# Kernel tuning notes

Measured on AMD Instinct MI355X. Metric: run time of the kernel, lower is better.

## Reference

```python
import jax, jax.numpy as jnp
import numpy as np

N = 100_000      # num_nodes
E = 1_600_000    # num_edges (avg degree 16)
D = 64           # embedding_dim
L = 3            # num_layers


def setup_inputs() -> dict:
    key = jax.random.key(0)
    k1, k2 = jax.random.split(key)
    edge_index = jax.random.randint(k1, (2, E), 0, N, dtype=jnp.int64)
    edge_weight = jnp.ones((E,), jnp.float32)
    # nn.init.normal_(std=0.1)
    embedding = 0.1 * jax.random.normal(k2, (N, D), dtype=jnp.float32)
    return {"embedding": embedding, "edge_weight": edge_weight, "edge_index": edge_index}


def reference(embedding, edge_weight, edge_index):
    n = embedding.shape[0]
    self_idx = jnp.arange(n, dtype=edge_index.dtype)
    # add_self_loops: append (i, i) with weight 1 (PyG default fill_value)
    row = jnp.concatenate([edge_index[0], self_idx])  # source j
    col = jnp.concatenate([edge_index[1], self_idx])  # target i
    ew = jnp.concatenate([edge_weight, jnp.ones((n,), embedding.dtype)])
    # degree() counts occurrences of row (unweighted)
    deg = jax.ops.segment_sum(jnp.ones_like(ew), row, num_segments=n)
    deg_inv_sqrt = jnp.where(deg > 0, jax.lax.rsqrt(deg), 0.0)
    norm = deg_inv_sqrt[row] * ew * deg_inv_sqrt[col]  # [E+N]

    x = embedding
    acc = embedding  # running sum of layer-0..L embeddings
    for _ in range(L):
        # gather from source, scale, scatter-add to target (dropout off in eval)
        msg = norm[:, None] * x[row]                       # [E+N, D]
        x = jax.ops.segment_sum(msg, col, num_segments=n)  # [N, D]
        acc = acc + x
    return acc / (L + 1)
```

## Files before the change

### kernel.cpp

```cpp
#include <hip/hip_runtime.h>
#include <stdint.h>

#define DIM 64
#define BINS 20000
#define RANGES 5
#define NSLICE 51
#define TBH 512
#define SCAN_TILE 1024

__device__ __forceinline__ unsigned bf16rne(float f) {
    unsigned u = __float_as_uint(f);
    return (u + 0x7FFFu + ((u >> 16) & 1u)) >> 16;
}
__device__ __forceinline__ unsigned pack2(float lo, float hi) {
    return bf16rne(lo) | (bf16rne(hi) << 16);
}
#define UNPK(u, lo, hi) { lo = __uint_as_float((u) << 16); hi = __uint_as_float((u) & 0xFFFF0000u); }

__global__ void __launch_bounds__(TBH)
hist_kernel(const int* __restrict__ src, const int* __restrict__ dst,
            int* __restrict__ partialsA, int* __restrict__ partialsB,
            int* __restrict__ lrank, int E, int N, int Es) {
    __shared__ int h[BINS];
    const int b = blockIdx.x;
    const int kind = b / (RANGES * NSLICE);
    const int rs = b % (RANGES * NSLICE);
    const int r = rs / NSLICE, s = rs % NSLICE;
    const int base = r * BINS;
    const int hi = min(base + BINS, N);
    const int nb = hi - base;
    for (int j = threadIdx.x; j < nb; j += TBH) h[j] = 0;
    __syncthreads();
    const int e0 = s * Es, e1 = min(e0 + Es, E);
    if (kind == 0) {
#pragma unroll 4
        for (int i = e0 + threadIdx.x; i < e1; i += TBH) {
            unsigned j = (unsigned)(dst[i] - base);
            if (j < (unsigned)BINS) lrank[i] = atomicAdd(&h[j], 1);
        }
    } else {
#pragma unroll 4
        for (int i = e0 + threadIdx.x; i < e1; i += TBH) {
            unsigned j = (unsigned)(src[i] - base);
            if (j < (unsigned)BINS) atomicAdd(&h[j], 1);
        }
    }
    __syncthreads();
    int* part = (kind ? partialsB : partialsA) + (size_t)s * N + base;
    for (int j = threadIdx.x; j < nb; j += TBH) part[j] = h[j];
}

__global__ void __launch_bounds__(256)
merge_kernel(int* __restrict__ partialsA, const int* __restrict__ partialsB,
             int* __restrict__ indeg, float* __restrict__ dis, int N) {
    const int i = blockIdx.x * blockDim.x + threadIdx.x;
    if (i >= N) return;
    int run = 0;
    for (int s = 0; s < NSLICE; ++s) {
        int v = partialsA[(size_t)s * N + i];
        partialsA[(size_t)s * N + i] = run;
        run += v;
    }
    indeg[i] = run;
    int od = 0;
    for (int s = 0; s < NSLICE; ++s) od += partialsB[(size_t)s * N + i];
    dis[i] = rsqrtf((float)od + 1.0f);
}


__global__ void __launch_bounds__(256)
scan_partial(const int* __restrict__ indeg, int* __restrict__ partial, int n) {
    __shared__ int wsum[4];
    const int tid = threadIdx.x;
    const int base = blockIdx.x * SCAN_TILE + tid * 4;
    int s = 0;
    if (base + 3 < n) {
        int4 v = *(const int4*)(indeg + base);
        s = v.x + v.y + v.z + v.w;
    } else {
        for (int i = 0; i < 4; ++i) if (base + i < n) s += indeg[base + i];
    }
    for (int off = 32; off > 0; off >>= 1) s += __shfl_down(s, off, 64);
    const int lane = tid & 63, wid = tid >> 6;
    if (lane == 0) wsum[wid] = s;
    __syncthreads();
    if (tid == 0) partial[blockIdx.x] = wsum[0] + wsum[1] + wsum[2] + wsum[3];
}

__global__ void scan_blocksums(int* __restrict__ partial, int* __restrict__ offsets,
                               int nblocks, int n) {
    __shared__ int buf[1024];
    const int t = threadIdx.x;
    int v = (t < nblocks) ? partial[t] : 0;
    buf[t] = v;
    __syncthreads();
    for (int off = 1; off < 1024; off <<= 1) {
        int add = (t >= off) ? buf[t - off] : 0;
        __syncthreads();
        buf[t] += add;
        __syncthreads();
    }
    if (t < nblocks) partial[t] = buf[t] - v;
    if (t == 1023) offsets[n] = buf[1023];
}

__global__ void __launch_bounds__(256)
scan_final(const int* __restrict__ indeg, const int* __restrict__ partial,
           int* __restrict__ offsets, int n) {
    __shared__ int wpre[4];
    const int tid = threadIdx.x;
    const int base = blockIdx.x * SCAN_TILE + tid * 4;
    int v0 = 0, v1 = 0, v2 = 0, v3 = 0;
    if (base + 3 < n) {
        int4 v = *(const int4*)(indeg + base);
        v0 = v.x; v1 = v.y; v2 = v.z; v3 = v.w;
    } else {
        if (base + 0 < n) v0 = indeg[base + 0];
        if (base + 1 < n) v1 = indeg[base + 1];
        if (base + 2 < n) v2 = indeg[base + 2];
        if (base + 3 < n) v3 = indeg[base + 3];
    }
    const int s = v0 + v1 + v2 + v3;
    int inc = s;
    const int lane = tid & 63, wid = tid >> 6;
    for (int off = 1; off < 64; off <<= 1) {
        int t = __shfl_up(inc, off, 64);
        if (lane >= off) inc += t;
    }
    if (lane == 63) wpre[wid] = inc;
    __syncthreads();
    if (tid == 0) {
        int r = 0;
        for (int w = 0; w < 4; ++w) { int t = wpre[w]; wpre[w] = r; r += t; }
    }
    __syncthreads();
    int run = (inc - s) + wpre[wid] + partial[blockIdx.x];
    if (base + 0 < n) { offsets[base + 0] = run; run += v0; }
    if (base + 1 < n) { offsets[base + 1] = run; run += v1; }
    if (base + 2 < n) { offsets[base + 2] = run; run += v2; }
    if (base + 3 < n) { offsets[base + 3] = run; run += v3; }
}

__global__ void fill_kernel(const int* __restrict__ src, const int* __restrict__ dst,
                            const float* __restrict__ ew, const float* __restrict__ dis,
                            const int* __restrict__ offsets, const int* __restrict__ sliceoff,
                            const int* __restrict__ lrank, int2* __restrict__ csr,
                            int E, int N, int Es) {
    const int i = blockIdx.x * blockDim.x + threadIdx.x;
    if (i < E) {
        const int s = i / Es;
        const int t = dst[i], sc = src[i];
        float w = dis[sc] * ew[i] * dis[t];
        int slot = offsets[t] + sliceoff[(size_t)s * N + t] + lrank[i];
        csr[slot] = make_int2(sc, __float_as_int(w));
    }
}

__global__ void __launch_bounds__(256)
conv_kernel(const float4* __restrict__ in4, uint4* __restrict__ outb, int n8) {
    int i = blockIdx.x * blockDim.x + threadIdx.x;
    if (i >= n8) return;
    float4 a = in4[2 * i], b = in4[2 * i + 1];
    uint4 o;
    o.x = pack2(a.x, a.y); o.y = pack2(a.z, a.w);
    o.z = pack2(b.x, b.y); o.w = pack2(b.z, b.w);
    outb[i] = o;
}

__global__ void __launch_bounds__(256)
prop_kernel(const uint4* __restrict__ xg, const float4* __restrict__ emb4,
            uint4* __restrict__ xstore, float4* __restrict__ out4,
            const int* __restrict__ offsets, const int2* __restrict__ csr,
            const float* __restrict__ dis, int n, int mode) {
    const int lane = threadIdx.x & 63;
    const int fl  = lane & 7;
    const int sub = lane >> 3;
    const int wave = blockIdx.x * (blockDim.x >> 6) + (threadIdx.x >> 6);
    const int node = wave * 8 + sub;
    if (node >= n) return;

    const int beg = offsets[node];
    const int end = offsets[node + 1];
    const float d = dis[node];
    const float dd = d * d;

    float a0, a1, a2, a3, a4, a5, a6, a7;
    float4 s0, s1;
    if (mode == 0) {
        s0 = emb4[node * 16 + fl * 2];
        s1 = emb4[node * 16 + fl * 2 + 1];
        a0 = dd * s0.x; a1 = dd * s0.y; a2 = dd * s0.z; a3 = dd * s0.w;
        a4 = dd * s1.x; a5 = dd * s1.y; a6 = dd * s1.z; a7 = dd * s1.w;
    } else {
        uint4 q = xg[(size_t)node * 8 + fl];
        float l, h;
        UNPK(q.x, l, h) a0 = dd * l; a1 = dd * h;
        UNPK(q.y, l, h) a2 = dd * l; a3 = dd * h;
        UNPK(q.z, l, h) a4 = dd * l; a5 = dd * h;
        UNPK(q.w, l, h) a6 = dd * l; a7 = dd * h;
    }

#define EDGE(E, Q) { float w_ = __int_as_float((E).y); float l, h; \
    UNPK((Q).x, l, h) a0 = fmaf(w_, l, a0); a1 = fmaf(w_, h, a1); \
    UNPK((Q).y, l, h) a2 = fmaf(w_, l, a2); a3 = fmaf(w_, h, a3); \
    UNPK((Q).z, l, h) a4 = fmaf(w_, l, a4); a5 = fmaf(w_, h, a5); \
    UNPK((Q).w, l, h) a6 = fmaf(w_, l, a6); a7 = fmaf(w_, h, a7); }

    int p = beg;
    for (; p + 4 <= end; p += 4) {
        int2 e0 = csr[p + 0], e1 = csr[p + 1], e2 = csr[p + 2], e3 = csr[p + 3];
        uint4 q0 = xg[(size_t)e0.x * 8 + fl];
        uint4 q1 = xg[(size_t)e1.x * 8 + fl];
        uint4 q2 = xg[(size_t)e2.x * 8 + fl];
        uint4 q3 = xg[(size_t)e3.x * 8 + fl];
        EDGE(e0, q0) EDGE(e1, q1) EDGE(e2, q2) EDGE(e3, q3)
    }
    for (; p < end; ++p) {
        int2 e = csr[p];
        uint4 q = xg[(size_t)e.x * 8 + fl];
        EDGE(e, q)
    }
#undef EDGE

    if (mode != 2) {
        uint4 o;
        o.x = pack2(a0, a1); o.y = pack2(a2, a3);
        o.z = pack2(a4, a5); o.w = pack2(a6, a7);
        xstore[(size_t)node * 8 + fl] = o;
    }
    const int oi = node * 16 + fl * 2;
    if (mode == 0) {
        out4[oi]     = make_float4(0.25f * (s0.x + a0), 0.25f * (s0.y + a1),
                                   0.25f * (s0.z + a2), 0.25f * (s0.w + a3));
        out4[oi + 1] = make_float4(0.25f * (s1.x + a4), 0.25f * (s1.y + a5),
                                   0.25f * (s1.z + a6), 0.25f * (s1.w + a7));
    } else {
        float4 p0 = out4[oi], p1 = out4[oi + 1];
        out4[oi]     = make_float4(fmaf(0.25f, a0, p0.x), fmaf(0.25f, a1, p0.y),
                                   fmaf(0.25f, a2, p0.z), fmaf(0.25f, a3, p0.w));
        out4[oi + 1] = make_float4(fmaf(0.25f, a4, p1.x), fmaf(0.25f, a5, p1.y),
                                   fmaf(0.25f, a6, p1.z), fmaf(0.25f, a7, p1.w));
    }
}


extern "C" void kernel_launch(void* const* d_in, const int* in_sizes, int n_in,
                              void* d_out, int out_size, void* d_ws, size_t ws_size,
                              hipStream_t stream) {
    const float* emb = (const float*)d_in[0];
    const float* ew  = (const float*)d_in[1];
    const int*   ei  = (const int*)d_in[2];
    const int E = in_sizes[2] / 2;
    const int N = in_sizes[0] / DIM;
    const int* src = ei;
    const int* dst = ei + E;
    float* out = (float*)d_out;

    const int Es = (E + NSLICE - 1) / NSLICE;
    const int nscan = (N + SCAN_TILE - 1) / SCAN_TILE;

    char* w = (char*)d_ws;
    int* partialsA = (int*)w; w += (size_t)NSLICE * N * 4;
    size_t unionSz = ((size_t)NSLICE * N * 4 + 255) & ~(size_t)255;
    int* partialsB = (int*)w;
    uint4* xb      = (uint4*)w; w += unionSz;
    int* lrank   = (int*)w;  w += (size_t)E * 4;
    int* indeg   = (int*)w;  w += (size_t)N * 4;
    int* offsets = (int*)w;  w += (size_t)(N + 1) * 4;
    float* dis   = (float*)w; w += (size_t)N * 4;
    int* partial = (int*)w;  w += (size_t)1024 * 4;
    w = (char*)(((uintptr_t)w + 255) & ~(uintptr_t)255);
    int2* csr    = (int2*)w; w += (size_t)E * 8;
    w = (char*)(((uintptr_t)w + 255) & ~(uintptr_t)255);
    uint4* x0c   = (uint4*)w; w += (size_t)N * DIM * 2;
    uint4* xa    = (uint4*)w; w += (size_t)N * DIM * 2;

    const int TB = 256;
    hist_kernel<<<2 * RANGES * NSLICE, TBH, 0, stream>>>(src, dst, partialsA, partialsB,
                                                         lrank, E, N, Es);
    merge_kernel<<<(N + TB - 1) / TB, TB, 0, stream>>>(partialsA, partialsB,
                                                       indeg, dis, N);
    scan_partial<<<nscan, TB, 0, stream>>>(indeg, partial, N);
    scan_blocksums<<<1, 1024, 0, stream>>>(partial, offsets, nscan, N);
    scan_final<<<nscan, TB, 0, stream>>>(indeg, partial, offsets, N);
    fill_kernel<<<(E + TB - 1) / TB, TB, 0, stream>>>(src, dst, ew, dis, offsets,
                                                      partialsA, lrank, csr, E, N, Es);
    const int n8 = N * DIM / 8;
    conv_kernel<<<(n8 + TB - 1) / TB, TB, 0, stream>>>((const float4*)emb, x0c, n8);

    dim3 grid((N + 31) / 32), block(TB);
    prop_kernel<<<grid, block, 0, stream>>>(x0c, (const float4*)emb, xa, (float4*)out,
                                            offsets, csr, dis, N, 0);
    prop_kernel<<<grid, block, 0, stream>>>(xa, nullptr, xb, (float4*)out,
                                            offsets, csr, dis, N, 1);
    prop_kernel<<<grid, block, 0, stream>>>(xb, nullptr, nullptr, (float4*)out,
                                            offsets, csr, dis, N, 2);
}
```

Baseline: 316.7 us.

## Pack histogram bins and slice partials as 16-bit counters, vectorize CSR fill

The histogram now keeps two 16-bit counters per 32-bit shared-memory word, so one block covers 50000 nodes. That cuts the node ranges from 5 to 2, raises slices to 64 and threads per block to 1024, and reduces redundant scans of the edge list. The per-slice partial counts and local ranks are stored as unsigned short, halving the workspace traffic in the histogram, merge and fill kernels. The fill kernel processes four edges per thread with vector loads. The risk is 16-bit overflow if a node receives 65536 or more edges within one slice or in total, and more atomic contention on packed words.

```diff
diff --git a/kernel.cpp b/kernel.cpp
--- a/kernel.cpp
+++ b/kernel.cpp
@@ -2,10 +2,10 @@
 #include <stdint.h>
 
 #define DIM 64
-#define BINS 20000
-#define RANGES 5
-#define NSLICE 51
-#define TBH 512
+#define BINS2 50000
+#define RANGES 2
+#define NSLICE 64
+#define TBH 1024
 #define SCAN_TILE 1024
 
 __device__ __forceinline__ unsigned bf16rne(float f) {
@@ -19,46 +19,50 @@
 
 __global__ void __launch_bounds__(TBH)
 hist_kernel(const int* __restrict__ src, const int* __restrict__ dst,
-            int* __restrict__ partialsA, int* __restrict__ partialsB,
-            int* __restrict__ lrank, int E, int N, int Es) {
-    __shared__ int h[BINS];
+            unsigned short* __restrict__ partialsA, unsigned short* __restrict__ partialsB,
+            unsigned short* __restrict__ lrank, int E, int N, int Es) {
+    __shared__ unsigned h32[BINS2 / 2];
     const int b = blockIdx.x;
     const int kind = b / (RANGES * NSLICE);
     const int rs = b % (RANGES * NSLICE);
     const int r = rs / NSLICE, s = rs % NSLICE;
-    const int base = r * BINS;
-    const int hi = min(base + BINS, N);
-    const int nb = hi - base;
-    for (int j = threadIdx.x; j < nb; j += TBH) h[j] = 0;
+    const int base = r * BINS2;
+    const int hi = min(base + BINS2, N);
+    const int nbw = (hi - base + 1) >> 1;
+    for (int j = threadIdx.x; j < nbw; j += TBH) h32[j] = 0;
     __syncthreads();
     const int e0 = s * Es, e1 = min(e0 + Es, E);
     if (kind == 0) {
 #pragma unroll 4
         for (int i = e0 + threadIdx.x; i < e1; i += TBH) {
             unsigned j = (unsigned)(dst[i] - base);
-            if (j < (unsigned)BINS) lrank[i] = atomicAdd(&h[j], 1);
+            if (j < (unsigned)BINS2) {
+                const unsigned sh = (j & 1) * 16;
+                unsigned old = atomicAdd(&h32[j >> 1], 1u << sh);
+                lrank[i] = (unsigned short)((old >> sh) & 0xFFFFu);
+            }
         }
     } else {
 #pragma unroll 4
         for (int i = e0 + threadIdx.x; i < e1; i += TBH) {
             unsigned j = (unsigned)(src[i] - base);
-            if (j < (unsigned)BINS) atomicAdd(&h[j], 1);
+            if (j < (unsigned)BINS2) atomicAdd(&h32[j >> 1], 1u << ((j & 1) * 16));
         }
     }
     __syncthreads();
-    int* part = (kind ? partialsB : partialsA) + (size_t)s * N + base;
-    for (int j = threadIdx.x; j < nb; j += TBH) part[j] = h[j];
-}
-
-__global__ void __launch_bounds__(256)
-merge_kernel(int* __restrict__ partialsA, const int* __restrict__ partialsB,
+    unsigned* part = (unsigned*)((kind ? partialsB : partialsA) + (size_t)s * N + base);
+    for (int j = threadIdx.x; j < nbw; j += TBH) part[j] = h32[j];
+}
+
+__global__ void __launch_bounds__(256)
+merge_kernel(unsigned short* __restrict__ partialsA, const unsigned short* __restrict__ partialsB,
              int* __restrict__ indeg, float* __restrict__ dis, int N) {
     const int i = blockIdx.x * blockDim.x + threadIdx.x;
     if (i >= N) return;
     int run = 0;
     for (int s = 0; s < NSLICE; ++s) {
         int v = partialsA[(size_t)s * N + i];
-        partialsA[(size_t)s * N + i] = run;
+        partialsA[(size_t)s * N + i] = (unsigned short)run;
         run += v;
     }
     indeg[i] = run;
@@ -141,18 +145,36 @@
     if (base + 3 < n) { offsets[base + 3] = run; run += v3; }
 }
 
-__global__ void fill_kernel(const int* __restrict__ src, const int* __restrict__ dst,
-                            const float* __restrict__ ew, const float* __restrict__ dis,
-                            const int* __restrict__ offsets, const int* __restrict__ sliceoff,
-                            const int* __restrict__ lrank, int2* __restrict__ csr,
-                            int E, int N, int Es) {
-    const int i = blockIdx.x * blockDim.x + threadIdx.x;
-    if (i < E) {
-        const int s = i / Es;
-        const int t = dst[i], sc = src[i];
-        float w = dis[sc] * ew[i] * dis[t];
-        int slot = offsets[t] + sliceoff[(size_t)s * N + t] + lrank[i];
-        csr[slot] = make_int2(sc, __float_as_int(w));
+__global__ void __launch_bounds__(256)
+fill_kernel(const int* __restrict__ src, const int* __restrict__ dst,
+            const float* __restrict__ ew, const float* __restrict__ dis,
+            const int* __restrict__ offsets, const unsigned short* __restrict__ sliceoff,
+            const unsigned short* __restrict__ lrank, int2* __restrict__ csr,
+            int E, int N, int Es) {
+    const int i0 = (blockIdx.x * blockDim.x + threadIdx.x) * 4;
+    if (i0 + 3 < E) {
+        int4   ss = *(const int4*)(src + i0);
+        int4   tt = *(const int4*)(dst + i0);
+        float4 ww = *(const float4*)(ew + i0);
+        ushort4 lr = *(const ushort4*)(lrank + i0);
+        int sl = i0 / Es;
+#define DO(K, SF, TF, WF, LF) { int sE = (i0 + K) / Es; \
+        int slot = offsets[TF] + sliceoff[(size_t)sE * N + TF] + (int)(LF); \
+        csr[slot] = make_int2(SF, __float_as_int(dis[SF] * (WF) * dis[TF])); }
+        (void)sl;
+        DO(0, ss.x, tt.x, ww.x, lr.x)
+        DO(1, ss.y, tt.y, ww.y, lr.y)
+        DO(2, ss.z, tt.z, ww.z, lr.z)
+        DO(3, ss.w, tt.w, ww.w, lr.w)
+#undef DO
+    } else {
+        for (int i = i0; i < E; ++i) {
+            int sE = i / Es;
+            int t = dst[i], sc = src[i];
+            float w = dis[sc] * ew[i] * dis[t];
+            int slot = offsets[t] + sliceoff[(size_t)sE * N + t] + (int)lrank[i];
+            csr[slot] = make_int2(sc, __float_as_int(w));
+        }
     }
 }
 
@@ -260,11 +282,14 @@
     const int nscan = (N + SCAN_TILE - 1) / SCAN_TILE;
 
     char* w = (char*)d_ws;
-    int* partialsA = (int*)w; w += (size_t)NSLICE * N * 4;
-    size_t unionSz = ((size_t)NSLICE * N * 4 + 255) & ~(size_t)255;
-    int* partialsB = (int*)w;
-    uint4* xb      = (uint4*)w; w += unionSz;
-    int* lrank   = (int*)w;  w += (size_t)E * 4;
+    unsigned short* partialsA = (unsigned short*)w; w += (size_t)NSLICE * N * 2;
+    size_t unionSz = (size_t)NSLICE * N * 2;
+    size_t xbSz = (size_t)N * DIM * 2;
+    if (xbSz > unionSz) unionSz = xbSz;
+    unionSz = (unionSz + 255) & ~(size_t)255;
+    unsigned short* partialsB = (unsigned short*)w;
+    uint4* xb = (uint4*)w; w += unionSz;
+    unsigned short* lrank = (unsigned short*)w; w += (size_t)E * 2;
     int* indeg   = (int*)w;  w += (size_t)N * 4;
     int* offsets = (int*)w;  w += (size_t)(N + 1) * 4;
     float* dis   = (float*)w; w += (size_t)N * 4;
@@ -283,8 +308,9 @@
     scan_partial<<<nscan, TB, 0, stream>>>(indeg, partial, N);
     scan_blocksums<<<1, 1024, 0, stream>>>(partial, offsets, nscan, N);
     scan_final<<<nscan, TB, 0, stream>>>(indeg, partial, offsets, N);
-    fill_kernel<<<(E + TB - 1) / TB, TB, 0, stream>>>(src, dst, ew, dis, offsets,
-                                                      partialsA, lrank, csr, E, N, Es);
+    const int e4 = (E + 3) / 4;
+    fill_kernel<<<(e4 + TB - 1) / TB, TB, 0, stream>>>(src, dst, ew, dis, offsets,
+                                                       partialsA, lrank, csr, E, N, Es);
     const int n8 = N * DIM / 8;
     conv_kernel<<<(n8 + TB - 1) / TB, TB, 0, stream>>>((const float4*)emb, x0c, n8);
 
```

Result: faster. 285.3 us (-9.9%).
